# Kernel optimization log

Measured on AMD Instinct MI355X. Metric: run time of the kernel, lower is better.

The kernel has to match this reference:

```python
import jax, jax.numpy as jnp
import numpy as np
from jax import lax

K = 13  # sizearea
DN = ('NCHW', 'OIHW', 'NCHW')


def conv(x, W, b):
    y = lax.conv_general_dilated(x, W, (1, 1), 'SAME', dimension_numbers=DN)
    return y + b[None, :, None, None]


def setup_inputs() -> dict:
    key = jax.random.key(0)
    ks = jax.random.split(key, 4)
    x = jax.random.normal(ks[0], (8, 1, 256, 256), dtype=jnp.float32)
    W1 = jax.random.normal(ks[1], (64, 1, 3, 3), dtype=jnp.float32) * 0.1
    b1 = jnp.zeros((64,), dtype=jnp.float32)
    W2 = jax.random.normal(ks[2], (64, 64, 3, 3), dtype=jnp.float32) * 0.05
    b2 = jnp.zeros((64,), dtype=jnp.float32)
    W3 = jax.random.normal(ks[3], (K * K, 64, 3, 3), dtype=jnp.float32) * 0.05
    b3 = jnp.zeros((K * K,), dtype=jnp.float32)
    return {'x': x, 'W1': W1, 'b1': b1, 'W2': W2, 'b2': b2, 'W3': W3, 'b3': b3}


def reference(x, W1, b1, W2, b2, W3, b3):
    # weight-predicting CNN (sar_data=False -> x used directly)
    h = jax.nn.relu(conv(x, W1, b1))
    h = jax.nn.relu(conv(h, W2, b2))
    w = conv(h, W3, b3)                       # (B, K*K, H, W)

    B, C, H, Wd = x.shape                     # C == 1
    # w.permute(0,2,3,1).view(B,1,H,W,K,K)
    wr = jnp.transpose(w, (0, 2, 3, 1)).reshape(B, 1, H, Wd, K, K)

    Ho, Wo = H - K + 1, Wd - K + 1            # unfold with stride 1, no pad
    pr, pc = (H - Ho) // 2, (Wd - Wo) // 2    # center-crop of weight maps
    wc = wr[:, :, pr:H - pr, pc:Wd - pc]      # (B,1,Ho,Wo,K,K)

    # patches[b,0,i,j,u,v] = x[b,0,i+u,j+v]  (C=1, so channel-major flatten is just (kh,kw))
    patches = lax.conv_general_dilated_patches(
        x, (K, K), (1, 1), 'VALID', dimension_numbers=DN)   # (B, K*K, Ho, Wo)
    patches = patches.reshape(B, 1, K, K, Ho, Wo).transpose(0, 1, 4, 5, 2, 3)

    # per-pixel weighted sum over the KxK window
    y = jnp.einsum('bchwuv,bchwuv->bchw', patches, wc)       # (B,1,Ho,Wo)
    return y
```

## Files before the change

### kernel.cpp

```cpp
#include <hip/hip_runtime.h>

#define HW 256
#define BATCH 8
#define C 64
#define HO 244
#define NPAD 192
#define KTOT 576

typedef __bf16 bf16x8 __attribute__((ext_vector_type(8)));
typedef float f32x16 __attribute__((ext_vector_type(16)));
typedef float f32x2 __attribute__((ext_vector_type(2)));
typedef unsigned short us8 __attribute__((ext_vector_type(8)));

__device__ inline unsigned short fbf(float f) {
    return __builtin_bit_cast(unsigned short, (__bf16)f);
}

__device__ inline float bf2f(unsigned short s) {
    union { unsigned int u; float f; } c;
    c.u = ((unsigned int)s) << 16;
    return c.f;
}

__global__ __launch_bounds__(256) void repack_w_kernel(
    const float* __restrict__ W2, const float* __restrict__ W3,
    unsigned short* __restrict__ B2g, unsigned short* __restrict__ B3g)
{
    int idx = blockIdx.x * 256 + threadIdx.x;
    if (idx < 36 * 2 * C * 8) {
        int e = idx & 7;
        int r = idx >> 3;
        int n = r & 63;
        int s = r >> 6;
        int khalf = s & 1;
        int kstep = s >> 1;
        int chunk = kstep >> 2, ks = kstep & 3;
        int ci = ks * 16 + khalf * 8 + e;
        B2g[idx] = fbf(W2[((size_t)n * C + ci) * 9 + chunk]);
    } else {
        int j = idx - 36 * 2 * C * 8;
        if (j >= 36 * 2 * NPAD * 8) return;
        int e = j & 7;
        int r = j >> 3;
        int n = r % NPAD;
        int s = r / NPAD;
        int khalf = s & 1;
        int kstep = s >> 1;
        int chunk = kstep >> 2, ks = kstep & 3;
        int ci = ks * 16 + khalf * 8 + e;
        float v = (n < 169) ? W3[((size_t)n * C + ci) * 9 + chunk] : 0.f;
        B3g[j] = fbf(v);
    }
}

__global__ __launch_bounds__(256, 3) void conv2_fused_kernel(
    const float* __restrict__ x, const float* __restrict__ W1,
    const float* __restrict__ b1, const unsigned short* __restrict__ W2r,
    const float* __restrict__ b2, unsigned short* __restrict__ h2)
{
    __shared__ unsigned short Ash[396 * 66];
    __shared__ unsigned short Xsh[8 * 68];

    const int t = threadIdx.x;
    const int lane = t & 63;
    const int wave = t >> 6;
    const int b  = blockIdx.z;
    const int h0 = blockIdx.y * 4;
    const int w0 = blockIdx.x * 64;

    const int col   = lane & 31;
    const int khalf = lane >> 5;
    const int mrow_base = wave * 64;

    const float* __restrict__ xplane = x + ((size_t)b << 16);
#pragma unroll
    for (int it = 0; it < 3; ++it) {
        int li = it * 256 + t;
        if (li < 8 * 68) {
            int rr = li / 68, cc = li - rr * 68;
            int hh = h0 - 2 + rr, ww = w0 - 2 + cc;
            bool ok = (hh >= 0) && (hh < HW) && (ww >= 0) && (ww < HW);
            Xsh[li] = ok ? fbf(xplane[hh * HW + ww]) : (unsigned short)0;
        }
    }

    const int g4 = t & 15;
    f32x2 w01[9], w23[9];
    f32x2 bia01, bia23;
    bia01[0] = b1[g4 * 4 + 0]; bia01[1] = b1[g4 * 4 + 1];
    bia23[0] = b1[g4 * 4 + 2]; bia23[1] = b1[g4 * 4 + 3];
#pragma unroll
    for (int q = 0; q < 9; ++q) {
        w01[q][0] = W1[(g4 * 4 + 0) * 9 + q];
        w01[q][1] = W1[(g4 * 4 + 1) * 9 + q];
        w23[q][0] = W1[(g4 * 4 + 2) * 9 + q];
        w23[q][1] = W1[(g4 * 4 + 3) * 9 + q];
    }

    __syncthreads();

    for (int it = 0; it < 25; ++it) {
        int li = it * 256 + t;
        if (li < 6336) {
            int p = li >> 4;
            int pr = p / 66, pc = p - pr * 66;
            int hh = h0 - 1 + pr, ww = w0 - 1 + pc;
            unsigned short ov[4];
            if (hh >= 0 && hh < HW && ww >= 0 && ww < HW) {
                const unsigned short* xb = Xsh + pr * 68 + pc;
                f32x2 a01 = bia01, a23 = bia23;
#pragma unroll
                for (int i = 0; i < 3; ++i)
#pragma unroll
                    for (int j = 0; j < 3; ++j) {
                        float xv = bf2f(xb[i * 68 + j]);
                        f32x2 xv2; xv2[0] = xv; xv2[1] = xv;
                        a01 += xv2 * w01[i * 3 + j];
                        a23 += xv2 * w23[i * 3 + j];
                    }
                ov[0] = fbf(fmaxf(a01[0], 0.f));
                ov[1] = fbf(fmaxf(a01[1], 0.f));
                ov[2] = fbf(fmaxf(a23[0], 0.f));
                ov[3] = fbf(fmaxf(a23[1], 0.f));
            } else {
#pragma unroll
                for (int u = 0; u < 4; ++u) ov[u] = 0;
            }
            *(uint2*)(Ash + p * 66 + g4 * 4) = *(uint2*)ov;
        }
    }

    const unsigned short* bbase = W2r + ((size_t)khalf * C + col) * 8;
    us8 bc0 = *(const us8*)(bbase);
    us8 bc1 = *(const us8*)(bbase + 32 * 8);

    f32x16 acc[2][2];
#pragma unroll
    for (int ai = 0; ai < 2; ++ai)
#pragma unroll
        for (int nb = 0; nb < 2; ++nb)
#pragma unroll
            for (int r = 0; r < 16; ++r) acc[ai][nb][r] = 0.f;

    __syncthreads();

#pragma unroll
    for (int chunk = 0; chunk < 9; ++chunk) {
        const int ii = chunk / 3, jj = chunk - ii * 3;
        const int pixbase = (wave + ii) * 66 + jj;
#pragma unroll
        for (int ks = 0; ks < 4; ++ks) {
            const int kstep = chunk * 4 + ks;
            us8 bn0, bn1;
            if (kstep < 35) {
                const unsigned short* bp = bbase + (size_t)(kstep + 1) * (2 * C * 8);
                bn0 = *(const us8*)(bp);
                bn1 = *(const us8*)(bp + 32 * 8);
            }
            const int koff = ks * 16 + khalf * 8;
            bf16x8 a0 = __builtin_bit_cast(bf16x8, *(const us8*)(Ash + (pixbase + col) * 66 + koff));
            bf16x8 a1 = __builtin_bit_cast(bf16x8, *(const us8*)(Ash + (pixbase + col + 32) * 66 + koff));
            bf16x8 v0 = __builtin_bit_cast(bf16x8, bc0);
            bf16x8 v1 = __builtin_bit_cast(bf16x8, bc1);
            acc[0][0] = __builtin_amdgcn_mfma_f32_32x32x16_bf16(a0, v0, acc[0][0], 0, 0, 0);
            acc[0][1] = __builtin_amdgcn_mfma_f32_32x32x16_bf16(a0, v1, acc[0][1], 0, 0, 0);
            acc[1][0] = __builtin_amdgcn_mfma_f32_32x32x16_bf16(a1, v0, acc[1][0], 0, 0, 0);
            acc[1][1] = __builtin_amdgcn_mfma_f32_32x32x16_bf16(a1, v1, acc[1][1], 0, 0, 0);
            bc0 = bn0; bc1 = bn1;
        }
    }

#pragma unroll
    for (int nb = 0; nb < 2; ++nb) {
        const int n = nb * 32 + col;
        const float bias = b2[n];
#pragma unroll
        for (int ai = 0; ai < 2; ++ai) {
#pragma unroll
            for (int r = 0; r < 16; ++r) {
                int m = mrow_base + ai * 32 + (r & 3) + ((r >> 2) << 3) + (khalf << 2);
                int h = h0 + (m >> 6), w = w0 + (m & 63);
                float val = fmaxf(acc[ai][nb][r] + bias, 0.f);
                h2[(((size_t)b * HW + h) * HW + w) * C + n] = fbf(val);
            }
        }
    }
}

__global__ __launch_bounds__(512, 3) void conv3_mfma_kernel(
    const float* __restrict__ x, const unsigned short* __restrict__ h2,
    const unsigned short* __restrict__ Bg, const float* __restrict__ b3,
    float* __restrict__ y)
{
    __shared__ unsigned short Ash[396 * 72];
    __shared__ float Xsh[16 * 77];
    __shared__ float red[8][64];

    const int t = threadIdx.x;
    const int lane = t & 63;
    const int wave = t >> 6;
    const int b   = blockIdx.z;
    const int ho0 = blockIdx.y * 4;
    const int wo0 = blockIdx.x * 64;

    const int col   = lane & 31;
    const int khalf = lane >> 5;
    const int rsel      = wave >> 1;
    const int mrow_base = rsel * 64;
    const int nbase     = (wave & 1) * 96;

    f32x16 acc[2][3];
#pragma unroll
    for (int mi = 0; mi < 2; ++mi)
#pragma unroll
        for (int ni = 0; ni < 3; ++ni)
#pragma unroll
            for (int r = 0; r < 16; ++r) acc[mi][ni][r] = 0.f;

#pragma unroll
    for (int it = 0; it < 7; ++it) {
        int li = it * 512 + t;
        if (li < 396 * 8) {
            int p = li >> 3, g = li & 7;
            int row = p / 66, cl = p - row * 66;
            int ww = wo0 + 5 + cl; ww = ww < 255 ? ww : 255;
            size_t src = (((size_t)b * HW + (ho0 + 5 + row)) * HW + ww) * C + g * 8;
            *(uint4*)(Ash + p * 72 + g * 8) = *(const uint4*)(h2 + src);
        }
    }
    {
        const float* __restrict__ xplane = x + ((size_t)b << 16);
#pragma unroll
        for (int it = 0; it < 3; ++it) {
            int li = it * 512 + t;
            if (li < 16 * 76) {
                int rr = li / 76, cc = li - rr * 76;
                int ww = wo0 + cc; ww = ww < 255 ? ww : 255;
                Xsh[rr * 77 + cc] = xplane[(ho0 + rr) * HW + ww];
            }
        }
    }

    const unsigned short* bbase = Bg + ((size_t)khalf * NPAD + nbase + col) * 8;
    us8 bc0 = *(const us8*)(bbase);
    us8 bc1 = *(const us8*)(bbase + 32 * 8);
    us8 bc2 = *(const us8*)(bbase + 64 * 8);

    __syncthreads();

#pragma unroll
    for (int chunk = 0; chunk < 9; ++chunk) {
        const int ii = chunk / 3, jj = chunk - ii * 3;
        const int pixbase = (rsel + ii) * 66 + jj;
#pragma unroll
        for (int ks = 0; ks < 4; ++ks) {
            const int kstep = chunk * 4 + ks;
            us8 bn0, bn1, bn2;
            if (kstep < 35) {
                const unsigned short* bp = bbase + (size_t)(kstep + 1) * (2 * NPAD * 8);
                bn0 = *(const us8*)(bp);
                bn1 = *(const us8*)(bp + 32 * 8);
                bn2 = *(const us8*)(bp + 64 * 8);
            }
            const int koff = ks * 16 + khalf * 8;
            bf16x8 a0 = __builtin_bit_cast(bf16x8, *(const us8*)(Ash + (pixbase + col) * 72 + koff));
            bf16x8 a1 = __builtin_bit_cast(bf16x8, *(const us8*)(Ash + (pixbase + col + 32) * 72 + koff));
            bf16x8 v0 = __builtin_bit_cast(bf16x8, bc0);
            bf16x8 v1 = __builtin_bit_cast(bf16x8, bc1);
            bf16x8 v2 = __builtin_bit_cast(bf16x8, bc2);
            acc[0][0] = __builtin_amdgcn_mfma_f32_32x32x16_bf16(a0, v0, acc[0][0], 0, 0, 0);
            acc[0][1] = __builtin_amdgcn_mfma_f32_32x32x16_bf16(a0, v1, acc[0][1], 0, 0, 0);
            acc[0][2] = __builtin_amdgcn_mfma_f32_32x32x16_bf16(a0, v2, acc[0][2], 0, 0, 0);
            acc[1][0] = __builtin_amdgcn_mfma_f32_32x32x16_bf16(a1, v0, acc[1][0], 0, 0, 0);
            acc[1][1] = __builtin_amdgcn_mfma_f32_32x32x16_bf16(a1, v1, acc[1][1], 0, 0, 0);
            acc[1][2] = __builtin_amdgcn_mfma_f32_32x32x16_bf16(a1, v2, acc[1][2], 0, 0, 0);
            bc0 = bn0; bc1 = bn1; bc2 = bn2;
        }
    }

    int   qv[3], uo[3], vo[3];
    float b3v[3];
#pragma unroll
    for (int ni = 0; ni < 3; ++ni) {
        int q = nbase + ni * 32 + col;
        qv[ni] = q;
        int u = q / 13;
        uo[ni] = u;
        vo[ni] = q - u * 13;
        b3v[ni] = (q < 169) ? b3[q] : 0.f;
    }

    float partial[2][16];
#pragma unroll
    for (int mi = 0; mi < 2; ++mi)
#pragma unroll
        for (int r = 0; r < 16; ++r) {
            int mrow = mi * 32 + (r & 3) + ((r >> 2) << 3) + (khalf << 2);
            bool wok = (wo0 + mrow) < HO;
            float p = 0.f;
#pragma unroll
            for (int ni = 0; ni < 3; ++ni) {
                if (qv[ni] < 169 && wok) {
                    float s = acc[mi][ni][r] + b3v[ni];
                    p += s * Xsh[(rsel + uo[ni]) * 77 + mrow + vo[ni]];
                }
            }
            partial[mi][r] = p;
        }

#pragma unroll
    for (int mi = 0; mi < 2; ++mi)
#pragma unroll
        for (int r = 0; r < 16; ++r) {
            float p = partial[mi][r];
#pragma unroll
            for (int d = 1; d < 32; d <<= 1) p += __shfl_xor(p, d, 64);
            partial[mi][r] = p;
        }

    if (col == 0) {
#pragma unroll
        for (int mi = 0; mi < 2; ++mi)
#pragma unroll
            for (int r = 0; r < 16; ++r) {
                int mrow = mi * 32 + (r & 3) + ((r >> 2) << 3) + (khalf << 2);
                red[wave][mrow] = partial[mi][r];
            }
    }
    __syncthreads();

    if (t < 256) {
        int row_sel = t >> 6, m = t & 63;
        float val = red[row_sel * 2][m] + red[row_sel * 2 + 1][m];
        int wo = wo0 + m, ho = ho0 + row_sel;
        if (wo < HO)
            y[((size_t)b * HO + ho) * HO + wo] = val;
    }
}

extern "C" void kernel_launch(void* const* d_in, const int* in_sizes, int n_in,
                              void* d_out, int out_size, void* d_ws, size_t ws_size,
                              hipStream_t stream) {
    const float* x  = (const float*)d_in[0];
    const float* W1 = (const float*)d_in[1];
    const float* b1 = (const float*)d_in[2];
    const float* W2 = (const float*)d_in[3];
    const float* b2 = (const float*)d_in[4];
    const float* W3 = (const float*)d_in[5];
    const float* b3 = (const float*)d_in[6];
    float* out = (float*)d_out;

    unsigned short* h2  = (unsigned short*)d_ws;
    unsigned short* W2r = h2 + (size_t)BATCH * HW * HW * C;
    unsigned short* W3r = W2r + (size_t)36 * 2 * C * 8;

    repack_w_kernel<<<576, 256, 0, stream>>>(W2, W3, W2r, W3r);
    conv2_fused_kernel<<<dim3(4, 64, 8), 256, 0, stream>>>(x, W1, b1, W2r, b2, h2);
    conv3_mfma_kernel<<<dim3(4, 61, 8), 512, 0, stream>>>(x, h2, W3r, b3, out);
}
```

Baseline: 242.1 us.

## Halve conv2 tile height and split output channels across waves for occupancy

Result: slower. 249.5 us (+3.0%).

```diff
diff --git a/kernel.cpp b/kernel.cpp
--- a/kernel.cpp
+++ b/kernel.cpp
@@ -53,30 +53,38 @@
     }
 }
 
-__global__ __launch_bounds__(256, 3) void conv2_fused_kernel(
+__global__ __launch_bounds__(256, 4) void conv2_fused_kernel(
     const float* __restrict__ x, const float* __restrict__ W1,
     const float* __restrict__ b1, const unsigned short* __restrict__ W2r,
     const float* __restrict__ b2, unsigned short* __restrict__ h2)
 {
-    __shared__ unsigned short Ash[396 * 66];
-    __shared__ unsigned short Xsh[8 * 68];
+    __shared__ unsigned short Ash[264 * 66];
+    __shared__ unsigned short Xsh[6 * 68];
 
     const int t = threadIdx.x;
     const int lane = t & 63;
     const int wave = t >> 6;
     const int b  = blockIdx.z;
-    const int h0 = blockIdx.y * 4;
+    const int h0 = blockIdx.y * 2;
     const int w0 = blockIdx.x * 64;
 
     const int col   = lane & 31;
     const int khalf = lane >> 5;
-    const int mrow_base = wave * 64;
+    const int rsel      = wave >> 1;
+    const int mrow_base = rsel * 64;
+    const int nbase     = (wave & 1) * 32;
 
     const float* __restrict__ xplane = x + ((size_t)b << 16);
-#pragma unroll
-    for (int it = 0; it < 3; ++it) {
-        int li = it * 256 + t;
-        if (li < 8 * 68) {
+    {
+        int li = t;
+        if (li < 6 * 68) {
+            int rr = li / 68, cc = li - rr * 68;
+            int hh = h0 - 2 + rr, ww = w0 - 2 + cc;
+            bool ok = (hh >= 0) && (hh < HW) && (ww >= 0) && (ww < HW);
+            Xsh[li] = ok ? fbf(xplane[hh * HW + ww]) : (unsigned short)0;
+        }
+        li = 256 + t;
+        if (li < 6 * 68) {
             int rr = li / 68, cc = li - rr * 68;
             int hh = h0 - 2 + rr, ww = w0 - 2 + cc;
             bool ok = (hh >= 0) && (hh < HW) && (ww >= 0) && (ww < HW);
@@ -99,9 +107,9 @@
 
     __syncthreads();
 
-    for (int it = 0; it < 25; ++it) {
+    for (int it = 0; it < 17; ++it) {
         int li = it * 256 + t;
-        if (li < 6336) {
+        if (li < 4224) {
             int p = li >> 4;
             int pr = p / 66, pc = p - pr * 66;
             int hh = h0 - 1 + pr, ww = w0 - 1 + pc;
@@ -130,49 +138,36 @@
         }
     }
 
-    const unsigned short* bbase = W2r + ((size_t)khalf * C + col) * 8;
-    us8 bc0 = *(const us8*)(bbase);
-    us8 bc1 = *(const us8*)(bbase + 32 * 8);
-
-    f32x16 acc[2][2];
+    const unsigned short* bbase = W2r + ((size_t)khalf * C + nbase + col) * 8;
+    us8 bc = *(const us8*)(bbase);
+
+    f32x16 acc[2];
 #pragma unroll
     for (int ai = 0; ai < 2; ++ai)
 #pragma unroll
-        for (int nb = 0; nb < 2; ++nb)
-#pragma unroll
-            for (int r = 0; r < 16; ++r) acc[ai][nb][r] = 0.f;
+        for (int r = 0; r < 16; ++r) acc[ai][r] = 0.f;
 
     __syncthreads();
 
 #pragma unroll
-    for (int chunk = 0; chunk < 9; ++chunk) {
+    for (int kstep = 0; kstep < 36; ++kstep) {
+        const int chunk = kstep >> 2, ks = kstep & 3;
         const int ii = chunk / 3, jj = chunk - ii * 3;
-        const int pixbase = (wave + ii) * 66 + jj;
-#pragma unroll
-        for (int ks = 0; ks < 4; ++ks) {
-            const int kstep = chunk * 4 + ks;
-            us8 bn0, bn1;
-            if (kstep < 35) {
-                const unsigned short* bp = bbase + (size_t)(kstep + 1) * (2 * C * 8);
-                bn0 = *(const us8*)(bp);
-                bn1 = *(const us8*)(bp + 32 * 8);
-            }
-            const int koff = ks * 16 + khalf * 8;
-            bf16x8 a0 = __builtin_bit_cast(bf16x8, *(const us8*)(Ash + (pixbase + col) * 66 + koff));
-            bf16x8 a1 = __builtin_bit_cast(bf16x8, *(const us8*)(Ash + (pixbase + col + 32) * 66 + koff));
-            bf16x8 v0 = __builtin_bit_cast(bf16x8, bc0);
-            bf16x8 v1 = __builtin_bit_cast(bf16x8, bc1);
-            acc[0][0] = __builtin_amdgcn_mfma_f32_32x32x16_bf16(a0, v0, acc[0][0], 0, 0, 0);
-            acc[0][1] = __builtin_amdgcn_mfma_f32_32x32x16_bf16(a0, v1, acc[0][1], 0, 0, 0);
-            acc[1][0] = __builtin_amdgcn_mfma_f32_32x32x16_bf16(a1, v0, acc[1][0], 0, 0, 0);
-            acc[1][1] = __builtin_amdgcn_mfma_f32_32x32x16_bf16(a1, v1, acc[1][1], 0, 0, 0);
-            bc0 = bn0; bc1 = bn1;
-        }
-    }
-
-#pragma unroll
-    for (int nb = 0; nb < 2; ++nb) {
-        const int n = nb * 32 + col;
+        const int pixbase = (rsel + ii) * 66 + jj;
+        us8 bn;
+        if (kstep + 1 < 36)
+            bn = *(const us8*)(bbase + (size_t)(kstep + 1) * (2 * C * 8));
+        const int koff = ks * 16 + khalf * 8;
+        bf16x8 a0 = __builtin_bit_cast(bf16x8, *(const us8*)(Ash + (pixbase + col) * 66 + koff));
+        bf16x8 a1 = __builtin_bit_cast(bf16x8, *(const us8*)(Ash + (pixbase + col + 32) * 66 + koff));
+        bf16x8 bv = __builtin_bit_cast(bf16x8, bc);
+        acc[0] = __builtin_amdgcn_mfma_f32_32x32x16_bf16(a0, bv, acc[0], 0, 0, 0);
+        acc[1] = __builtin_amdgcn_mfma_f32_32x32x16_bf16(a1, bv, acc[1], 0, 0, 0);
+        bc = bn;
+    }
+
+    {
+        const int n = nbase + col;
         const float bias = b2[n];
 #pragma unroll
         for (int ai = 0; ai < 2; ++ai) {
@@ -180,7 +175,7 @@
             for (int r = 0; r < 16; ++r) {
                 int m = mrow_base + ai * 32 + (r & 3) + ((r >> 2) << 3) + (khalf << 2);
                 int h = h0 + (m >> 6), w = w0 + (m & 63);
-                float val = fmaxf(acc[ai][nb][r] + bias, 0.f);
+                float val = fmaxf(acc[ai][r] + bias, 0.f);
                 h2[(((size_t)b * HW + h) * HW + w) * C + n] = fbf(val);
             }
         }
@@ -249,33 +244,30 @@
     __syncthreads();
 
 #pragma unroll
-    for (int chunk = 0; chunk < 9; ++chunk) {
+    for (int kstep = 0; kstep < 36; ++kstep) {
+        const int chunk = kstep >> 2, ks = kstep & 3;
         const int ii = chunk / 3, jj = chunk - ii * 3;
         const int pixbase = (rsel + ii) * 66 + jj;
-#pragma unroll
-        for (int ks = 0; ks < 4; ++ks) {
-            const int kstep = chunk * 4 + ks;
-            us8 bn0, bn1, bn2;
-            if (kstep < 35) {
-                const unsigned short* bp = bbase + (size_t)(kstep + 1) * (2 * NPAD * 8);
-                bn0 = *(const us8*)(bp);
-                bn1 = *(const us8*)(bp + 32 * 8);
-                bn2 = *(const us8*)(bp + 64 * 8);
-            }
-            const int koff = ks * 16 + khalf * 8;
-            bf16x8 a0 = __builtin_bit_cast(bf16x8, *(const us8*)(Ash + (pixbase + col) * 72 + koff));
-            bf16x8 a1 = __builtin_bit_cast(bf16x8, *(const us8*)(Ash + (pixbase + col + 32) * 72 + koff));
-            bf16x8 v0 = __builtin_bit_cast(bf16x8, bc0);
-            bf16x8 v1 = __builtin_bit_cast(bf16x8, bc1);
-            bf16x8 v2 = __builtin_bit_cast(bf16x8, bc2);
-            acc[0][0] = __builtin_amdgcn_mfma_f32_32x32x16_bf16(a0, v0, acc[0][0], 0, 0, 0);
-            acc[0][1] = __builtin_amdgcn_mfma_f32_32x32x16_bf16(a0, v1, acc[0][1], 0, 0, 0);
-            acc[0][2] = __builtin_amdgcn_mfma_f32_32x32x16_bf16(a0, v2, acc[0][2], 0, 0, 0);
-            acc[1][0] = __builtin_amdgcn_mfma_f32_32x32x16_bf16(a1, v0, acc[1][0], 0, 0, 0);
-            acc[1][1] = __builtin_amdgcn_mfma_f32_32x32x16_bf16(a1, v1, acc[1][1], 0, 0, 0);
-            acc[1][2] = __builtin_amdgcn_mfma_f32_32x32x16_bf16(a1, v2, acc[1][2], 0, 0, 0);
-            bc0 = bn0; bc1 = bn1; bc2 = bn2;
-        }
+        us8 bn0, bn1, bn2;
+        if (kstep + 1 < 36) {
+            const unsigned short* bp = bbase + (size_t)(kstep + 1) * (2 * NPAD * 8);
+            bn0 = *(const us8*)(bp);
+            bn1 = *(const us8*)(bp + 32 * 8);
+            bn2 = *(const us8*)(bp + 64 * 8);
+        }
+        const int koff = ks * 16 + khalf * 8;
+        bf16x8 a0 = __builtin_bit_cast(bf16x8, *(const us8*)(Ash + (pixbase + col) * 72 + koff));
+        bf16x8 a1 = __builtin_bit_cast(bf16x8, *(const us8*)(Ash + (pixbase + col + 32) * 72 + koff));
+        bf16x8 v0 = __builtin_bit_cast(bf16x8, bc0);
+        bf16x8 v1 = __builtin_bit_cast(bf16x8, bc1);
+        bf16x8 v2 = __builtin_bit_cast(bf16x8, bc2);
+        acc[0][0] = __builtin_amdgcn_mfma_f32_32x32x16_bf16(a0, v0, acc[0][0], 0, 0, 0);
+        acc[0][1] = __builtin_amdgcn_mfma_f32_32x32x16_bf16(a0, v1, acc[0][1], 0, 0, 0);
+        acc[0][2] = __builtin_amdgcn_mfma_f32_32x32x16_bf16(a0, v2, acc[0][2], 0, 0, 0);
+        acc[1][0] = __builtin_amdgcn_mfma_f32_32x32x16_bf16(a1, v0, acc[1][0], 0, 0, 0);
+        acc[1][1] = __builtin_amdgcn_mfma_f32_32x32x16_bf16(a1, v1, acc[1][1], 0, 0, 0);
+        acc[1][2] = __builtin_amdgcn_mfma_f32_32x32x16_bf16(a1, v2, acc[1][2], 0, 0, 0);
+        bc0 = bn0; bc1 = bn1; bc2 = bn2;
     }
 
     int   qv[3], uo[3], vo[3];
@@ -355,6 +347,6 @@
     unsigned short* W3r = W2r + (size_t)36 * 2 * C * 8;
 
     repack_w_kernel<<<576, 256, 0, stream>>>(W2, W3, W2r, W3r);
-    conv2_fused_kernel<<<dim3(4, 64, 8), 256, 0, stream>>>(x, W1, b1, W2r, b2, h2);
+    conv2_fused_kernel<<<dim3(4, 128, 8), 256, 0, stream>>>(x, W1, b1, W2r, b2, h2);
     conv3_mfma_kernel<<<dim3(4, 61, 8), 512, 0, stream>>>(x, h2, W3r, b3, out);
 }
```
